# Kernel optimization log

Measured on AMD Instinct MI355X. Metric: run time of the kernel, lower is better.

Reference implementation:

```python
import jax, jax.numpy as jnp
import numpy as np

B, S, D, H = 4, 4096, 1024, 64


def setup_inputs() -> dict:
    key = jax.random.key(0)
    k1, k2, k3, k4 = jax.random.split(key, 4)
    x = jax.random.normal(k1, (B, S, D), dtype=jnp.float32)
    # nn.Linear(D, H, bias=False) weights, stored as [D, H] for x @ W
    scale = 1.0 / np.sqrt(D)
    Wk = jax.random.uniform(k2, (D, H), dtype=jnp.float32, minval=-scale, maxval=scale)
    Wq = jax.random.uniform(k3, (D, H), dtype=jnp.float32, minval=-scale, maxval=scale)
    Wv = jax.random.uniform(k4, (D, H), dtype=jnp.float32, minval=-scale, maxval=scale)
    return {"x": x, "Wq": Wq, "Wk": Wk, "Wv": Wv}


def reference(x, Wq, Wk, Wv):
    # x: [B, S, D]
    head_size = Wq.shape[-1]
    q = jnp.einsum('bsd,dh->bsh', x, Wq)
    k = jnp.einsum('bsd,dh->bsh', x, Wk)
    v = jnp.einsum('bsd,dh->bsh', x, Wv)
    scores = jnp.einsum('bqh,bkh->bqk', q, k) * (head_size ** -0.5)  # [B,S,S]
    S_ = x.shape[1]
    causal = jnp.tril(jnp.ones((S_, S_), dtype=bool))
    scores = jnp.where(causal[None, :, :], scores, -jnp.inf)
    attn = jax.nn.softmax(scores, axis=-1)
    return jnp.einsum('bqk,bkh->bqh', attn, v)  # [B,S,H]
```

## Files before the change

kernel.cpp:

```cpp
#include <hip/hip_runtime.h>

typedef __attribute__((ext_vector_type(8))) short bf16x8;
typedef __attribute__((ext_vector_type(4))) float f32x4;

#define MFMA16(A, Bv, C) __builtin_amdgcn_mfma_f32_16x16x32_bf16((A), (Bv), (C), 0, 0, 0)
#define WAITVM(N) asm volatile("s_waitcnt vmcnt(" #N ")" ::: "memory")

static constexpr int NB = 4, NS = 4096, ND = 1024, NH = 64;

__device__ __forceinline__ unsigned short f2bf(float f) {
    union { float f; unsigned int u; } x; x.f = f;
    unsigned int r = x.u + 0x7fffu + ((x.u >> 16) & 1u);
    return (unsigned short)(r >> 16);
}

__device__ __forceinline__ void gload_lds16(const void* g, void* l) {
    __builtin_amdgcn_global_load_lds((const __attribute__((address_space(1))) void*)g,
                                     (__attribute__((address_space(3))) void*)l, 16, 0, 0);
}

__global__ __launch_bounds__(256) void wconv(
    const float* __restrict__ Wq, const float* __restrict__ Wk,
    const float* __restrict__ Wv, unsigned short* __restrict__ wT)
{
    int mn = blockIdx.x;
    int m = mn >> 6, n = mn & 63;
    const float* W = (m == 0) ? Wq : (m == 1) ? Wk : Wv;
    unsigned short* dst = wT + (size_t)mn * ND;
    for (int k = threadIdx.x; k < ND; k += 256)
        dst[k] = f2bf(W[(size_t)k * NH + n]);
}

__global__ __launch_bounds__(256) void qkv_proj(
    const float* __restrict__ x, const unsigned short* __restrict__ wT,
    unsigned short* __restrict__ qo, unsigned short* __restrict__ ko,
    unsigned short* __restrict__ vt)
{
    __shared__ unsigned short Ws[4][192][32];
    __shared__ float Xs[4][32][32];
    __shared__ unsigned short Ls[32][72];

    const int tid  = threadIdx.x;
    const int lane = tid & 63;
    const int w    = tid >> 6;
    const int lr   = lane & 15;
    const int lg   = lane >> 4;
    const int rf   = w & 1;
    const int cg   = w >> 1;
    const int mbase = blockIdx.x * 32;

    const int srow = lane >> 2;
    const int schk = (lane & 3) ^ (srow & 3);
    const int xrow = lane >> 3;
    const int xchk = (lane & 7) ^ ((xrow & 3) << 1);

    f32x4 acc[6];
    #pragma unroll
    for (int i = 0; i < 6; ++i) acc[i] = (f32x4){0.f, 0.f, 0.f, 0.f};

    #define STAGE(slot, kt)                                                          \
        do {                                                                         \
            _Pragma("unroll")                                                        \
            for (int i_ = 0; i_ < 3; ++i_) {                                         \
                int rbase_ = w * 48 + i_ * 16;                                       \
                const unsigned short* src_ =                                         \
                    wT + (size_t)(rbase_ + srow) * ND + (kt) * 32 + schk * 8;        \
                gload_lds16(src_, &Ws[slot][rbase_][0]);                             \
            }                                                                        \
            {                                                                        \
                const float* xsrc_ =                                                 \
                    x + (size_t)(mbase + w * 8 + xrow) * ND + (kt) * 32 + xchk * 4;  \
                gload_lds16(xsrc_, &Xs[slot][w * 8][0]);                             \
            }                                                                        \
        } while (0)

    STAGE(0, 0);
    STAGE(1, 1);
    STAGE(2, 2);

    const int xg = (lg ^ (lr & 3)) * 8;
    for (int kt = 0; kt < 32; ++kt) {
        __builtin_amdgcn_sched_barrier(0);
        if (kt < 30)       WAITVM(8);
        else if (kt == 30) WAITVM(4);
        else               WAITVM(0);
        __builtin_amdgcn_s_barrier();
        __builtin_amdgcn_sched_barrier(0);
        if (kt + 3 < 32) STAGE((kt + 3) & 3, kt + 3);

        const int slot = kt & 3;
        float4 u0 = *(const float4*)&Xs[slot][rf * 16 + lr][xg];
        float4 u1 = *(const float4*)&Xs[slot][rf * 16 + lr][xg + 4];
        bf16x8 a;
        a[0] = (short)f2bf(u0.x); a[1] = (short)f2bf(u0.y);
        a[2] = (short)f2bf(u0.z); a[3] = (short)f2bf(u0.w);
        a[4] = (short)f2bf(u1.x); a[5] = (short)f2bf(u1.y);
        a[6] = (short)f2bf(u1.z); a[7] = (short)f2bf(u1.w);

        #pragma unroll
        for (int m = 0; m < 3; ++m)
            #pragma unroll
            for (int fi = 0; fi < 2; ++fi) {
                int row = m * 64 + (cg * 2 + fi) * 16 + lr;
                bf16x8 bfr = *(const bf16x8*)&Ws[slot][row][((lg ^ (lr & 3))) * 8];
                acc[m * 2 + fi] = MFMA16(a, bfr, acc[m * 2 + fi]);
            }
    }

    #pragma unroll
    for (int fi = 0; fi < 2; ++fi)
        #pragma unroll
        for (int r = 0; r < 4; ++r) {
            int srw = lg * 4 + r;
            int col = (cg * 2 + fi) * 16 + lr;
            size_t grow = (size_t)(mbase + rf * 16 + srw);
            qo[grow * NH + col] = f2bf(acc[fi][r] * 0.125f);
            ko[grow * NH + col] = f2bf(acc[2 + fi][r]);
            Ls[rf * 16 + srw][col] = f2bf(acc[4 + fi][r]);
        }
    __syncthreads();
    {
        int h  = tid >> 2;
        int so = (tid & 3) * 8;
        unsigned short tmp[8];
        #pragma unroll
        for (int jj = 0; jj < 8; ++jj) tmp[jj] = Ls[so + jj][h];
        int b_ = mbase >> 12;
        int sb = (mbase & (NS - 1)) + so;
        unsigned short* dst = vt + ((size_t)(b_ * NH + h)) * NS + sb;
        bf16x8 v0;
        #pragma unroll
        for (int jj = 0; jj < 8; ++jj) v0[jj] = (short)tmp[jj];
        *(bf16x8*)dst = v0;
    }
    #undef STAGE
}

__global__ __launch_bounds__(256) void attn_part(
    const unsigned short* __restrict__ q, const unsigned short* __restrict__ k,
    const unsigned short* __restrict__ vt, float* __restrict__ pO,
    float* __restrict__ pm, float* __restrict__ pl)
{
    __shared__ unsigned short Kt[2][64][64];
    __shared__ unsigned short Vt[2][64][64];
    __shared__ unsigned short Ps[4][16][72];

    const int bid = blockIdx.x;
    const int b = bid & 3;
    const int j = (bid >> 2) & 63;
    const int c = bid >> 8;
    if (c > (j >> 3)) return;
    const int ntile = (j + 1 - c * 8 < 8) ? (j + 1 - c * 8) : 8;
    const int tg0 = c * 8;

    const int tid  = threadIdx.x;
    const int lane = tid & 63;
    const int w    = tid >> 6;
    const int lr   = lane & 15;
    const int lg   = lane >> 4;
    const size_t bq = (size_t)b * NS;
    const int qb = j * 64;

    const int srow = lane >> 3;
    const int schk = (lane & 7) ^ srow;

    #define STAGEKV(buf, tg)                                                          \
        do {                                                                          \
            int kvb_ = (tg) * 64;                                                     \
            if (w < 2) {                                                              \
                _Pragma("unroll")                                                     \
                for (int i_ = 0; i_ < 4; ++i_) {                                      \
                    int rb_ = w * 32 + i_ * 8;                                        \
                    const unsigned short* src_ =                                      \
                        k + (bq + kvb_ + rb_ + srow) * NH + schk * 8;                 \
                    gload_lds16(src_, &Kt[buf][rb_][0]);                              \
                }                                                                     \
            } else {                                                                  \
                _Pragma("unroll")                                                     \
                for (int i_ = 0; i_ < 4; ++i_) {                                      \
                    int rb_ = (w - 2) * 32 + i_ * 8;                                  \
                    const unsigned short* src_ =                                      \
                        vt + ((size_t)(b * NH + rb_ + srow)) * NS + kvb_ + schk * 8;  \
                    gload_lds16(src_, &Vt[buf][rb_][0]);                              \
                }                                                                     \
            }                                                                         \
        } while (0)

    bf16x8 qf0, qf1;
    {
        const unsigned short* qp = q + (bq + qb + w * 16 + lr) * NH + lg * 8;
        qf0 = *(const bf16x8*)qp;
        qf1 = *(const bf16x8*)(qp + 32);
    }

    f32x4 O[4];
    #pragma unroll
    for (int i = 0; i < 4; ++i) O[i] = (f32x4){0.f, 0.f, 0.f, 0.f};
    float mrow = -3.0e38f, lsum = 0.f;

    STAGEKV(0, tg0);
    __syncthreads();

    int cur = 0;
    for (int t = 0; t < ntile; ++t) {
        const int tg = tg0 + t;
        STAGEKV(cur ^ 1, (t + 1 < ntile) ? tg + 1 : tg0);

        f32x4 sf[4];
        #pragma unroll
        for (int f = 0; f < 4; ++f) {
            f32x4 s = (f32x4){0.f, 0.f, 0.f, 0.f};
            int row = f * 16 + lr;
            bf16x8 kb0 = *(const bf16x8*)&Kt[cur][row][((lg    ) ^ (lr & 7)) * 8];
            bf16x8 kb1 = *(const bf16x8*)&Kt[cur][row][((lg + 4) ^ (lr & 7)) * 8];
            s = MFMA16(kb0, qf0, s);
            s = MFMA16(kb1, qf1, s);
            sf[f] = s;
        }

        if (tg == j) {
            #pragma unroll
            for (int f = 0; f < 4; ++f) {
                #pragma unroll
                for (int r = 0; r < 4; ++r) {
                    int kvl = f * 16 + lg * 4 + r;
                    int ql  = w * 16 + lr;
                    if (kvl > ql) sf[f][r] = -3.0e38f;
                }
            }
        }

        float pmx = fmaxf(fmaxf(fmaxf(sf[0][0], sf[0][1]), fmaxf(sf[0][2], sf[0][3])),
                          fmaxf(fmaxf(sf[1][0], sf[1][1]), fmaxf(sf[1][2], sf[1][3])));
        float pmx2 = fmaxf(fmaxf(fmaxf(sf[2][0], sf[2][1]), fmaxf(sf[2][2], sf[2][3])),
                           fmaxf(fmaxf(sf[3][0], sf[3][1]), fmaxf(sf[3][2], sf[3][3])));
        pmx = fmaxf(pmx, pmx2);
        pmx = fmaxf(pmx, __shfl_xor(pmx, 16));
        pmx = fmaxf(pmx, __shfl_xor(pmx, 32));
        float mnew = fmaxf(mrow, pmx);
        float corr = __expf(mrow - mnew);
        mrow = mnew;
        float rs = 0.f;
        #pragma unroll
        for (int f = 0; f < 4; ++f)
            #pragma unroll
            for (int r = 0; r < 4; ++r) {
                float p = __expf(sf[f][r] - mnew);
                sf[f][r] = p;
                rs += p;
            }
        rs += __shfl_xor(rs, 16);
        rs += __shfl_xor(rs, 32);
        lsum = lsum * corr + rs;
        #pragma unroll
        for (int hf = 0; hf < 4; ++hf) O[hf] *= corr;

        #pragma unroll
        for (int f = 0; f < 4; ++f)
            #pragma unroll
            for (int r = 0; r < 4; ++r)
                Ps[w][lr][f * 16 + lg * 4 + r] = f2bf(sf[f][r]);

        bf16x8 pb0 = *(const bf16x8*)&Ps[w][lr][lg * 8];
        bf16x8 pb1 = *(const bf16x8*)&Ps[w][lr][32 + lg * 8];

        #pragma unroll
        for (int hf = 0; hf < 4; ++hf) {
            int row = hf * 16 + lr;
            bf16x8 vb0 = *(const bf16x8*)&Vt[cur][row][((lg    ) ^ (lr & 7)) * 8];
            bf16x8 vb1 = *(const bf16x8*)&Vt[cur][row][((lg + 4) ^ (lr & 7)) * 8];
            O[hf] = MFMA16(vb0, pb0, O[hf]);
            O[hf] = MFMA16(vb1, pb1, O[hf]);
        }

        __syncthreads();
        cur ^= 1;
    }

    const int a8 = j >> 3, r8 = j & 7;
    const int pidx = b * 288 + (a8 + 1) * (4 * a8 + r8) + c;
    float* Po = pO + (size_t)pidx * 4096;
    #pragma unroll
    for (int hf = 0; hf < 4; ++hf)
        *(f32x4*)&Po[(w * 16 + lr) * 64 + hf * 16 + lg * 4] = O[hf];
    if (lane < 16) {
        pm[pidx * 64 + w * 16 + lane] = mrow;
        pl[pidx * 64 + w * 16 + lane] = lsum;
    }
    #undef STAGEKV
}

__global__ __launch_bounds__(256) void attn_merge(
    const float* __restrict__ pO, const float* __restrict__ pm,
    const float* __restrict__ pl, float* __restrict__ out)
{
    const int bid = blockIdx.x;
    const int b = bid & 3, j = bid >> 2;
    const int nch = (j >> 3) + 1;
    const int a8 = j >> 3, r8 = j & 7;
    const int pbase = b * 288 + (a8 + 1) * (4 * a8 + r8);
    const int tid = threadIdx.x;
    const int row = tid >> 2, hq = (tid & 3) * 16;

    float M = -3.0e38f, L = 0.f;
    f32x4 acc0 = {0,0,0,0}, acc1 = {0,0,0,0}, acc2 = {0,0,0,0}, acc3 = {0,0,0,0};
    for (int cc = 0; cc < nch; ++cc) {
        int pidx = pbase + cc;
        float mc = pm[pidx * 64 + row];
        float lc = pl[pidx * 64 + row];
        const f32x4* po = (const f32x4*)(pO + (size_t)pidx * 4096 + row * 64 + hq);
        float Mn = fmaxf(M, mc);
        float sO = __expf(M - Mn), sN = __expf(mc - Mn);
        L = L * sO + lc * sN;
        acc0 = acc0 * sO + po[0] * sN;
        acc1 = acc1 * sO + po[1] * sN;
        acc2 = acc2 * sO + po[2] * sN;
        acc3 = acc3 * sO + po[3] * sN;
        M = Mn;
    }
    float inv = 1.f / L;
    float* op = out + ((size_t)b * NS + (size_t)j * 64 + row) * NH + hq;
    *(f32x4*)(op + 0)  = acc0 * inv;
    *(f32x4*)(op + 4)  = acc1 * inv;
    *(f32x4*)(op + 8)  = acc2 * inv;
    *(f32x4*)(op + 12) = acc3 * inv;
}

extern "C" void kernel_launch(void* const* d_in, const int* in_sizes, int n_in,
                              void* d_out, int out_size, void* d_ws, size_t ws_size,
                              hipStream_t stream)
{
    const float* x  = (const float*)d_in[0];
    const float* Wq = (const float*)d_in[1];
    const float* Wk = (const float*)d_in[2];
    const float* Wv = (const float*)d_in[3];
    float* out = (float*)d_out;

    const size_t n = (size_t)NB * NS * NH;
    unsigned short* qb_ = (unsigned short*)d_ws;
    unsigned short* kb_ = qb_ + n;
    unsigned short* vT  = kb_ + n;
    unsigned short* wT  = vT + n;
    float* pO  = (float*)(wT + 192 * 1024);
    float* pm_ = pO + (size_t)1152 * 4096;
    float* pl_ = pm_ + 1152 * 64;

    wconv<<<dim3(192), dim3(256), 0, stream>>>(Wq, Wk, Wv, wT);
    qkv_proj<<<dim3(512), dim3(256), 0, stream>>>(x, wT, qb_, kb_, vT);
    attn_part<<<dim3(2048), dim3(256), 0, stream>>>(qb_, kb_, vT, pO, pm_, pl_);
    attn_merge<<<dim3(256), dim3(256), 0, stream>>>(pO, pm_, pl_, out);
}
```

Before: 71.45 us.

## Retile QKV projection to 64-row blocks with 512 threads and 64-wide K steps

The QKV projection kernel now processes 64 rows of x per block with 8 waves instead of 32 rows with 4, and stages 64-wide K chunks with triple buffering instead of 32-wide with quad buffering. Each wave computes a 32x48 output sub-tile and reuses each B fragment across two A row-fragments, so every W tile loaded is shared by twice as many rows of x. This halves redundant W traffic and cuts the number of barriers per block. In exchange it uses much more LDS per block, only 256 blocks are launched, and the XOR swizzles are new.

```diff
diff --git a/kernel.cpp b/kernel.cpp
--- a/kernel.cpp
+++ b/kernel.cpp
@@ -31,102 +31,119 @@
         dst[k] = f2bf(W[(size_t)k * NH + n]);
 }
 
-__global__ __launch_bounds__(256) void qkv_proj(
+__global__ __launch_bounds__(512) void qkv_proj(
     const float* __restrict__ x, const unsigned short* __restrict__ wT,
     unsigned short* __restrict__ qo, unsigned short* __restrict__ ko,
     unsigned short* __restrict__ vt)
 {
-    __shared__ unsigned short Ws[4][192][32];
-    __shared__ float Xs[4][32][32];
-    __shared__ unsigned short Ls[32][72];
+    __shared__ unsigned short Ws[3][192][64];
+    __shared__ float Xs[3][64][64];
+    __shared__ unsigned short Ls[64][72];
 
     const int tid  = threadIdx.x;
     const int lane = tid & 63;
     const int w    = tid >> 6;
     const int lr   = lane & 15;
     const int lg   = lane >> 4;
-    const int rf   = w & 1;
-    const int cg   = w >> 1;
-    const int mbase = blockIdx.x * 32;
-
-    const int srow = lane >> 2;
-    const int schk = (lane & 3) ^ (srow & 3);
-    const int xrow = lane >> 3;
-    const int xchk = (lane & 7) ^ ((xrow & 3) << 1);
+    const int mg   = w >> 2;
+    const int cg   = w & 3;
+    const int mbase = blockIdx.x * 64;
+
+    const int wr8 = lane >> 3;
+    const int wck = (lane & 7) ^ wr8;
+    const int xr4 = lane >> 4;
+    const int xck = lane & 15;
 
     f32x4 acc[6];
     #pragma unroll
     for (int i = 0; i < 6; ++i) acc[i] = (f32x4){0.f, 0.f, 0.f, 0.f};
 
-    #define STAGE(slot, kt)                                                          \
-        do {                                                                         \
-            _Pragma("unroll")                                                        \
-            for (int i_ = 0; i_ < 3; ++i_) {                                         \
-                int rbase_ = w * 48 + i_ * 16;                                       \
-                const unsigned short* src_ =                                         \
-                    wT + (size_t)(rbase_ + srow) * ND + (kt) * 32 + schk * 8;        \
-                gload_lds16(src_, &Ws[slot][rbase_][0]);                             \
-            }                                                                        \
-            {                                                                        \
-                const float* xsrc_ =                                                 \
-                    x + (size_t)(mbase + w * 8 + xrow) * ND + (kt) * 32 + xchk * 4;  \
-                gload_lds16(xsrc_, &Xs[slot][w * 8][0]);                             \
-            }                                                                        \
+    #define STAGE(slot, kb)                                                           \
+        do {                                                                          \
+            _Pragma("unroll")                                                         \
+            for (int i_ = 0; i_ < 3; ++i_) {                                          \
+                int rb_ = w * 24 + i_ * 8;                                            \
+                gload_lds16(wT + (size_t)(rb_ + wr8) * ND + (kb) + wck * 8,           \
+                            &Ws[slot][rb_][0]);                                       \
+            }                                                                         \
+            _Pragma("unroll")                                                         \
+            for (int j_ = 0; j_ < 2; ++j_) {                                          \
+                int rb_ = w * 8 + j_ * 4;                                             \
+                int r7_ = (rb_ + xr4) & 7;                                            \
+                gload_lds16(x + (size_t)(mbase + rb_ + xr4) * ND + (kb)               \
+                                + (xck ^ (r7_ << 1)) * 4,                             \
+                            &Xs[slot][rb_][0]);                                       \
+            }                                                                         \
         } while (0)
 
     STAGE(0, 0);
-    STAGE(1, 1);
-    STAGE(2, 2);
-
-    const int xg = (lg ^ (lr & 3)) * 8;
-    for (int kt = 0; kt < 32; ++kt) {
+    STAGE(1, 64);
+
+    for (int kt = 0; kt < 16; ++kt) {
         __builtin_amdgcn_sched_barrier(0);
-        if (kt < 30)       WAITVM(8);
-        else if (kt == 30) WAITVM(4);
-        else               WAITVM(0);
+        if (kt < 15) WAITVM(5);
+        else         WAITVM(0);
         __builtin_amdgcn_s_barrier();
         __builtin_amdgcn_sched_barrier(0);
-        if (kt + 3 < 32) STAGE((kt + 3) & 3, kt + 3);
-
-        const int slot = kt & 3;
-        float4 u0 = *(const float4*)&Xs[slot][rf * 16 + lr][xg];
-        float4 u1 = *(const float4*)&Xs[slot][rf * 16 + lr][xg + 4];
-        bf16x8 a;
-        a[0] = (short)f2bf(u0.x); a[1] = (short)f2bf(u0.y);
-        a[2] = (short)f2bf(u0.z); a[3] = (short)f2bf(u0.w);
-        a[4] = (short)f2bf(u1.x); a[5] = (short)f2bf(u1.y);
-        a[6] = (short)f2bf(u1.z); a[7] = (short)f2bf(u1.w);
-
-        #pragma unroll
-        for (int m = 0; m < 3; ++m)
-            #pragma unroll
-            for (int fi = 0; fi < 2; ++fi) {
-                int row = m * 64 + (cg * 2 + fi) * 16 + lr;
-                bf16x8 bfr = *(const bf16x8*)&Ws[slot][row][((lg ^ (lr & 3))) * 8];
-                acc[m * 2 + fi] = MFMA16(a, bfr, acc[m * 2 + fi]);
+        if (kt + 2 < 16) STAGE((kt + 2) % 3, (kt + 2) * 64);
+        __builtin_amdgcn_sched_barrier(0);
+
+        const int slot = kt % 3;
+        #pragma unroll
+        for (int sub = 0; sub < 2; ++sub) {
+            bf16x8 bfr[3];
+            #pragma unroll
+            for (int f = 0; f < 3; ++f) {
+                int row = cg * 48 + f * 16 + lr;
+                bfr[f] = *(const bf16x8*)&Ws[slot][row][(((sub << 2) | lg) ^ (lr & 7)) * 8];
             }
+            #pragma unroll
+            for (int a = 0; a < 2; ++a) {
+                int row = mg * 32 + a * 16 + lr;
+                const float* xp =
+                    &Xs[slot][row][((((sub << 3) | (lg << 1)) ^ ((lr & 7) << 1))) * 4];
+                float4 u0 = *(const float4*)xp;
+                float4 u1 = *(const float4*)(xp + 4);
+                bf16x8 af;
+                af[0] = (short)f2bf(u0.x); af[1] = (short)f2bf(u0.y);
+                af[2] = (short)f2bf(u0.z); af[3] = (short)f2bf(u0.w);
+                af[4] = (short)f2bf(u1.x); af[5] = (short)f2bf(u1.y);
+                af[6] = (short)f2bf(u1.z); af[7] = (short)f2bf(u1.w);
+                #pragma unroll
+                for (int f = 0; f < 3; ++f)
+                    acc[a * 3 + f] = MFMA16(af, bfr[f], acc[a * 3 + f]);
+            }
+        }
     }
 
     #pragma unroll
-    for (int fi = 0; fi < 2; ++fi)
-        #pragma unroll
-        for (int r = 0; r < 4; ++r) {
-            int srw = lg * 4 + r;
-            int col = (cg * 2 + fi) * 16 + lr;
-            size_t grow = (size_t)(mbase + rf * 16 + srw);
-            qo[grow * NH + col] = f2bf(acc[fi][r] * 0.125f);
-            ko[grow * NH + col] = f2bf(acc[2 + fi][r]);
-            Ls[rf * 16 + srw][col] = f2bf(acc[4 + fi][r]);
+    for (int a = 0; a < 2; ++a)
+        #pragma unroll
+        for (int f = 0; f < 3; ++f) {
+            int b16 = cg * 3 + f;
+            int sel = b16 >> 2;
+            int col = (b16 & 3) * 16 + lr;
+            #pragma unroll
+            for (int rr = 0; rr < 4; ++rr) {
+                int mrow = mg * 32 + a * 16 + lg * 4 + rr;
+                float v = acc[a * 3 + f][rr];
+                if (sel == 0)
+                    qo[(size_t)(mbase + mrow) * NH + col] = f2bf(v * 0.125f);
+                else if (sel == 1)
+                    ko[(size_t)(mbase + mrow) * NH + col] = f2bf(v);
+                else
+                    Ls[mrow][col] = f2bf(v);
+            }
         }
     __syncthreads();
     {
-        int h  = tid >> 2;
-        int so = (tid & 3) * 8;
+        int h  = tid >> 3;
+        int s8 = (tid & 7) * 8;
         unsigned short tmp[8];
         #pragma unroll
-        for (int jj = 0; jj < 8; ++jj) tmp[jj] = Ls[so + jj][h];
+        for (int jj = 0; jj < 8; ++jj) tmp[jj] = Ls[s8 + jj][h];
         int b_ = mbase >> 12;
-        int sb = (mbase & (NS - 1)) + so;
+        int sb = (mbase & (NS - 1)) + s8;
         unsigned short* dst = vt + ((size_t)(b_ * NH + h)) * NS + sb;
         bf16x8 v0;
         #pragma unroll
@@ -220,14 +237,13 @@
 
         if (tg == j) {
             #pragma unroll
-            for (int f = 0; f < 4; ++f) {
+            for (int f = 0; f < 4; ++f)
                 #pragma unroll
                 for (int r = 0; r < 4; ++r) {
                     int kvl = f * 16 + lg * 4 + r;
                     int ql  = w * 16 + lr;
                     if (kvl > ql) sf[f][r] = -3.0e38f;
                 }
-            }
         }
 
         float pmx = fmaxf(fmaxf(fmaxf(sf[0][0], sf[0][1]), fmaxf(sf[0][2], sf[0][3])),
@@ -346,7 +362,7 @@
     float* pl_ = pm_ + 1152 * 64;
 
     wconv<<<dim3(192), dim3(256), 0, stream>>>(Wq, Wk, Wv, wT);
-    qkv_proj<<<dim3(512), dim3(256), 0, stream>>>(x, wT, qb_, kb_, vT);
+    qkv_proj<<<dim3(256), dim3(512), 0, stream>>>(x, wT, qb_, kb_, vT);
     attn_part<<<dim3(2048), dim3(256), 0, stream>>>(qb_, kb_, vT, pO, pm_, pl_);
     attn_merge<<<dim3(256), dim3(256), 0, stream>>>(pO, pm_, pl_, out);
 }
```

Result: faster. 68.91 us (-3.6%).
